# Optimization experiments

Measured on AMD Instinct MI355X. Metric: run time of the kernel, lower is better.

## Reference

```python
import jax, jax.numpy as jnp
import numpy as np
from jax import lax


def _conv(x, w, padding):
    # NCHW input, OIHW weights, stride 1, no bias
    return lax.conv_general_dilated(x, w, (1, 1), padding,
                                    dimension_numbers=('NCHW', 'OIHW', 'NCHW'))


def setup_inputs() -> dict:
    key = jax.random.key(0)
    ks = jax.random.split(key, 6)
    B, C, H, W = 16, 512, 40, 40
    return {
        'exemplar': jax.random.normal(ks[0], (B, C, H, W), jnp.float32),
        'query':    jax.random.normal(ks[1], (B, C, H, W), jnp.float32),
        'w_e':  jax.random.normal(ks[2], (256, C, 1, 1), jnp.float32) * 0.01,
        'w_q':  jax.random.normal(ks[3], (256, C, 1, 1), jnp.float32) * 0.01,
        'w_c1': jax.random.normal(ks[4], (C, C, 3, 3), jnp.float32) * 0.01,
        'w_c2': jax.random.normal(ks[5], (C, C, 3, 3), jnp.float32) * 0.01,
    }


def reference(exemplar, query, w_e, w_q, w_c1, w_c2):
    B, C, H, W = query.shape
    N = H * W
    # 1x1 projections to 256-dim correlation space
    q_corr = _conv(query, w_q, 'VALID').reshape(B, -1, N)     # [B,256,N]
    e_corr = _conv(exemplar, w_e, 'VALID').reshape(B, -1, N)  # [B,256,N]
    # A[b, n_exemplar, m_query] = <e_corr[:, n], q_corr[:, m]>
    A = jnp.einsum('bcn,bcm->bnm', e_corr, q_corr)            # [B,N,N]
    # A1 = softmax over exemplar axis, then transpose (torch: softmax(A,dim=1).T)
    A1 = jnp.swapaxes(jax.nn.softmax(A, axis=1), 1, 2)        # [B,N,N]
    # Bm = softmax(A^T, dim=1).T  == softmax(A, axis=2)
    Bm = jnp.swapaxes(jax.nn.softmax(jnp.swapaxes(A, 1, 2), axis=1), 1, 2)
    e_flat = exemplar.reshape(B, C, N)
    q_flat = query.reshape(B, C, N)
    query_att = jnp.matmul(e_flat, A1)   # [B,C,N]
    exemplar_att = jnp.matmul(q_flat, Bm)  # [B,C,N]
    input1_att = _conv(exemplar_att.reshape(B, C, H, W), w_c1, 'SAME')
    input2_att = _conv(query_att.reshape(B, C, H, W), w_c2, 'SAME')
    return jnp.concatenate([input1_att, input2_att], axis=1)  # [B,2C,H,W]
```

## Files before the change

kernel.cpp:

```cpp
#include <hip/hip_runtime.h>

typedef unsigned short u16;
typedef __attribute__((ext_vector_type(8))) short bf16x8;
typedef __attribute__((ext_vector_type(4))) float f32x4;

__device__ __forceinline__ u16 f2bf(float f) {
  union { float f; unsigned u; } v; v.f = f;
  unsigned u = v.u;
  u += 0x7fffu + ((u >> 16) & 1u);
  return (u16)(u >> 16);
}

__device__ __forceinline__ void gll16(const void* g, void* l) {
  __builtin_amdgcn_global_load_lds(
      (const __attribute__((address_space(1))) void*)g,
      (__attribute__((address_space(3))) void*)l, 16, 0, 0);
}

__global__ __launch_bounds__(256) void transp_cast_x2(const float* __restrict__ ex,
                                                      const float* __restrict__ qu,
                                                      u16* __restrict__ xte,
                                                      u16* __restrict__ xtq) {
  __shared__ float t[32][33];
  int z = blockIdx.z;
  int b = z & 15;
  const float* xb = (z < 16 ? ex : qu) + (size_t)b * 819200;
  u16* xtb = (z < 16 ? xte : xtq) + (size_t)b * 819200;
  int n0 = blockIdx.x * 32, c0 = blockIdx.y * 32;
  int tx = threadIdx.x & 31, ty = threadIdx.x >> 5;
#pragma unroll
  for (int k = 0; k < 4; k++) {
    int c = ty + k * 8;
    t[c][tx] = xb[(size_t)(c0 + c) * 1600 + n0 + tx];
  }
  __syncthreads();
#pragma unroll
  for (int k = 0; k < 4; k++) {
    int n = ty + k * 8;
    xtb[(size_t)(n0 + n) * 512 + c0 + tx] = f2bf(t[tx][n]);
  }
}

__global__ void cast_w(const float* __restrict__ we, const float* __restrict__ wq,
                       u16* __restrict__ oe, u16* __restrict__ oq) {
  int i = blockIdx.x * 256 + threadIdx.x;
  oe[i] = f2bf(we[i]);
  oq[i] = f2bf(wq[i]);
}

__global__ void repack_wc(const float* __restrict__ w1, const float* __restrict__ w2,
                          u16* __restrict__ o1, u16* __restrict__ o2) {
  const float* w = blockIdx.y ? w2 : w1;
  u16* wr = blockIdx.y ? o2 : o1;
  int idx = blockIdx.x * 256 + threadIdx.x;
  int o = idx / 4608;
  int r = idx - o * 4608;
  int t = r >> 9;
  int c = r & 511;
  wr[idx] = f2bf(w[o * 4608 + c * 9 + t]);
}

__global__ void zero_mem(uint4* __restrict__ p, long n) {
  long i = (long)blockIdx.x * blockDim.x + threadIdx.x;
  long stride = (long)gridDim.x * blockDim.x;
  uint4 z; z.x = 0; z.y = 0; z.z = 0; z.w = 0;
  for (; i < n; i += stride) p[i] = z;
}

template <int MODE>
__global__ __launch_bounds__(256) void gemm_bt64(
    const u16* __restrict__ A, const u16* __restrict__ B, u16* __restrict__ C,
    const u16* __restrict__ A2, const u16* __restrict__ B2, u16* __restrict__ C2,
    int M, int N, int K, long sA, long sB, long sC) {
  __shared__ u16 lds_a[128 * 64];
  __shared__ u16 lds_b[128 * 64];
  int tid = threadIdx.x;
  int z = blockIdx.z, b = z & 15;
  const u16* Ab = (z < 16 ? A : A2) + (size_t)b * sA;
  const u16* Bb = (z < 16 ? B : B2) + (size_t)b * sB;
  u16* Cb = (z < 16 ? C : C2) + (size_t)b * sC;
  int m0 = blockIdx.x * 128, n0 = blockIdx.y * 128;

  int rsub = tid >> 3;
  int gch = (tid & 7) ^ (rsub & 7);
  long Kb = (long)K * 2;
  const char* pa[4];
  const char* pb[4];
#pragma unroll
  for (int c = 0; c < 4; c++) {
    int ra = m0 + 32 * c + rsub; ra = ra < M ? ra : M - 1;
    int rb = n0 + 32 * c + rsub; rb = rb < N ? rb : N - 1;
    pa[c] = (const char*)Ab + (long)ra * Kb + gch * 16;
    pb[c] = (const char*)Bb + (long)rb * Kb + gch * 16;
  }

  const f32x4 fzero = {0.f, 0.f, 0.f, 0.f};
  f32x4 acc[4][4];
#pragma unroll
  for (int mi = 0; mi < 4; mi++)
#pragma unroll
    for (int ni = 0; ni < 4; ni++) acc[mi][ni] = fzero;

  int wid = tid >> 6, lane = tid & 63;
  int wm = wid & 1, wn = wid >> 1;
  int lrow = lane & 15, lquad = lane >> 4;
  int sl = lrow & 7;

  int ksteps = K >> 6;
  for (int ks = 0; ks < ksteps; ks++) {
#pragma unroll
    for (int c = 0; c < 4; c++) {
      gll16(pa[c], (char*)lds_a + c * 4096 + tid * 16);
      gll16(pb[c], (char*)lds_b + c * 4096 + tid * 16);
      pa[c] += 128; pb[c] += 128;
    }
    __syncthreads();
#pragma unroll
    for (int k2 = 0; k2 < 2; k2++) {
      int sel = ((k2 << 2) | lquad) ^ sl;
      bf16x8 bv[4];
#pragma unroll
      for (int ni = 0; ni < 4; ni++) {
        int rowb = wn * 64 + ni * 16 + lrow;
        bv[ni] = *(const bf16x8*)((const char*)lds_b + rowb * 128 + sel * 16);
      }
#pragma unroll
      for (int mi = 0; mi < 4; mi++) {
        int rowa = wm * 64 + mi * 16 + lrow;
        bf16x8 av = *(const bf16x8*)((const char*)lds_a + rowa * 128 + sel * 16);
#pragma unroll
        for (int ni = 0; ni < 4; ni++)
          acc[mi][ni] =
              __builtin_amdgcn_mfma_f32_16x16x32_bf16(av, bv[ni], acc[mi][ni], 0, 0, 0);
      }
    }
    __syncthreads();
  }

#pragma unroll
  for (int mi = 0; mi < 4; mi++) {
#pragma unroll
    for (int r = 0; r < 4; r++) {
      int i = m0 + wm * 64 + mi * 16 + lquad * 4 + r;
      if (i >= M) continue;
#pragma unroll
      for (int ni = 0; ni < 4; ni++) {
        int j = n0 + wn * 64 + ni * 16 + lrow;
        if (j >= N) continue;
        Cb[(size_t)i * N + j] = f2bf(acc[mi][ni][r]);
      }
    }
  }
}

__global__ __launch_bounds__(256) void gemm_corr_exp(
    const u16* __restrict__ A, const u16* __restrict__ B, u16* __restrict__ E,
    u16* __restrict__ ET, float* __restrict__ Zrow, float* __restrict__ Zcol) {
  __shared__ u16 lds_a[128 * 64];
  __shared__ u16 lds_b[128 * 64];
  int tid = threadIdx.x;
  int b = blockIdx.z;
  const u16* Ab = A + (size_t)b * 409600;
  const u16* Bb = B + (size_t)b * 409600;
  u16* Eb = E + (size_t)b * 2560000;
  u16* ETb = ET + (size_t)b * 2560000;
  int m0 = blockIdx.x * 128, n0 = blockIdx.y * 128;

  int rsub = tid >> 3;
  int gch = (tid & 7) ^ (rsub & 7);
  const char* pa[4];
  const char* pb[4];
#pragma unroll
  for (int c = 0; c < 4; c++) {
    int ra = m0 + 32 * c + rsub; ra = ra < 1600 ? ra : 1599;
    int rb = n0 + 32 * c + rsub; rb = rb < 1600 ? rb : 1599;
    pa[c] = (const char*)(Ab + (size_t)ra * 256) + gch * 16;
    pb[c] = (const char*)(Bb + (size_t)rb * 256) + gch * 16;
  }

  const f32x4 fzero = {0.f, 0.f, 0.f, 0.f};
  f32x4 acc[4][4];
#pragma unroll
  for (int mi = 0; mi < 4; mi++)
#pragma unroll
    for (int ni = 0; ni < 4; ni++) acc[mi][ni] = fzero;

  int wid = tid >> 6, lane = tid & 63;
  int wm = wid & 1, wn = wid >> 1;
  int lrow = lane & 15, lquad = lane >> 4;
  int sl = lrow & 7;

  for (int ks = 0; ks < 4; ks++) {
#pragma unroll
    for (int c = 0; c < 4; c++) {
      gll16(pa[c], (char*)lds_a + c * 4096 + tid * 16);
      gll16(pb[c], (char*)lds_b + c * 4096 + tid * 16);
      pa[c] += 128; pb[c] += 128;
    }
    __syncthreads();
#pragma unroll
    for (int k2 = 0; k2 < 2; k2++) {
      int sel = ((k2 << 2) | lquad) ^ sl;
      bf16x8 bv[4];
#pragma unroll
      for (int ni = 0; ni < 4; ni++) {
        int rowb = wn * 64 + ni * 16 + lrow;
        bv[ni] = *(const bf16x8*)((const char*)lds_b + rowb * 128 + sel * 16);
      }
#pragma unroll
      for (int mi = 0; mi < 4; mi++) {
        int rowa = wm * 64 + mi * 16 + lrow;
        bf16x8 av = *(const bf16x8*)((const char*)lds_a + rowa * 128 + sel * 16);
#pragma unroll
        for (int ni = 0; ni < 4; ni++)
          acc[mi][ni] =
              __builtin_amdgcn_mfma_f32_16x16x32_bf16(av, bv[ni], acc[mi][ni], 0, 0, 0);
      }
    }
    __syncthreads();
  }

  const int TS = 136;
  u16* T = lds_a;
  float colacc[4] = {0.f, 0.f, 0.f, 0.f};
#pragma unroll
  for (int s = 0; s < 4; s++) {
    if (wm == (s >> 1)) {
      int smi0 = (s & 1) * 2;
#pragma unroll
      for (int mi2 = 0; mi2 < 2; mi2++) {
        int mi = smi0 + mi2;
        float rowp[4] = {0.f, 0.f, 0.f, 0.f};
#pragma unroll
        for (int ni = 0; ni < 4; ni++) {
          int j = n0 + wn * 64 + ni * 16 + lrow;
          bool jv = j < 1600;
#pragma unroll
          for (int r = 0; r < 4; r++) {
            int i = m0 + wm * 64 + mi * 16 + lquad * 4 + r;
            float e = __expf(acc[mi][ni][r]);
            T[(mi2 * 16 + lquad * 4 + r) * TS + wn * 64 + ni * 16 + lrow] = f2bf(e);
            rowp[r] += jv ? e : 0.f;
            colacc[ni] += (i < 1600) ? e : 0.f;
          }
        }
#pragma unroll
        for (int r = 0; r < 4; r++) {
          float v = rowp[r];
          v += __shfl_xor(v, 1);
          v += __shfl_xor(v, 2);
          v += __shfl_xor(v, 4);
          v += __shfl_xor(v, 8);
          int i = m0 + wm * 64 + mi * 16 + lquad * 4 + r;
          if (lrow == 0 && i < 1600) atomicAdd(&Zrow[b * 1600 + i], v);
        }
      }
    }
    __syncthreads();
#pragma unroll
    for (int p = 0; p < 2; p++) {
      int jj = tid + p * 256;
      int ml = jj >> 4, n8 = jj & 15;
      int gi = m0 + s * 32 + ml, gj = n0 + n8 * 8;
      if (gi < 1600 && gj < 1600)
        *(uint4*)(Eb + (size_t)gi * 1600 + gj) = *(const uint4*)&T[ml * TS + n8 * 8];
    }
#pragma unroll
    for (int p = 0; p < 4; p++) {
      int jj = tid + p * 256;
      int n = jj >> 3, m4 = jj & 7;
      int gm = m0 + s * 32 + m4 * 4, gn = n0 + n;
      if (gn < 1600 && gm < 1600) {
        ushort4 v;
        v.x = T[(m4 * 4 + 0) * TS + n];
        v.y = T[(m4 * 4 + 1) * TS + n];
        v.z = T[(m4 * 4 + 2) * TS + n];
        v.w = T[(m4 * 4 + 3) * TS + n];
        *(ushort4*)(ETb + (size_t)gn * 1600 + gm) = v;
      }
    }
    __syncthreads();
  }
#pragma unroll
  for (int ni = 0; ni < 4; ni++) {
    float v = colacc[ni];
    v += __shfl_xor(v, 16);
    v += __shfl_xor(v, 32);
    int j = n0 + wn * 64 + ni * 16 + lrow;
    if (lquad == 0 && j < 1600) atomicAdd(&Zcol[b * 1600 + j], v);
  }
}

__global__ void scale_div(const float* __restrict__ ex, const float* __restrict__ qu,
                          const float* __restrict__ Zcol, const float* __restrict__ Zrow,
                          u16* __restrict__ ebf, u16* __restrict__ qbf) {
  const float* x; const float* Z; u16* o;
  if (blockIdx.y == 0) { x = ex; Z = Zcol; o = ebf; }
  else { x = qu; Z = Zrow; o = qbf; }
  size_t idx = (size_t)blockIdx.x * 256 + threadIdx.x;
  int b = (int)(idx / 819200);
  int i = (int)(idx % 1600);
  o[idx] = f2bf(x[idx] / Z[b * 1600 + i]);
}


__global__ __launch_bounds__(256, 2) void att_gemm128(
    const u16* __restrict__ Aw1, const u16* __restrict__ Bp1, u16* __restrict__ C1,
    const u16* __restrict__ Aw2, const u16* __restrict__ Bp2, u16* __restrict__ C2) {
  __shared__ u16 ldsA[16384];
  __shared__ u16 ldsB[16384];
  int tid = threadIdx.x;
  int flat = blockIdx.x + blockIdx.y * 13 + blockIdx.z * 52;
  int wrk = (flat & 7) * 208 + (flat >> 3);
  int z = wrk / 52;
  int r2 = wrk - z * 52;
  int by = r2 / 13, bx = r2 - by * 13;
  int b = z & 15;
  const u16* Aw = (z < 16 ? Aw1 : Aw2) + (size_t)b * 819200;
  const u16* Bp = (z < 16 ? Bp1 : Bp2) + (size_t)b * 2560000;
  u16* Cb = (z < 16 ? C1 : C2) + (size_t)b * 903168;
  int p0 = bx * 128, c0 = by * 128;

  int rl = tid >> 2;
  int cs = (tid & 3) ^ ((rl >> 1) & 3);
  const char* pA0 = (const char*)(Aw + (size_t)(c0 + rl) * 1600) + cs * 16;
  const char* pA1 = pA0 + 64 * 3200;
  int pp0 = p0 + rl; pp0 = pp0 < 1600 ? pp0 : 1599;
  const char* pB0 = (const char*)(Bp + (size_t)pp0 * 1600) + cs * 16;
  int pp1 = p0 + 64 + rl; pp1 = pp1 < 1600 ? pp1 : 1599;
  const char* pB1 = (const char*)(Bp + (size_t)pp1 * 1600) + cs * 16;

  char* ldsAb = (char*)ldsA;
  char* ldsBb = (char*)ldsB;
  int dstT = tid * 16;

#define STAGE_U(d, kh, ks)                                              \
  {                                                                     \
    int ko = (ks) * 64;                                                 \
    int ro = ((d) * 2 + (kh)) * 8192;                                   \
    gll16(pA0 + ko, ldsAb + ro + dstT);                                 \
    gll16(pA1 + ko, ldsAb + ro + 4096 + dstT);                          \
    gll16(pB0 + ko, ldsBb + ro + dstT);                                 \
    gll16(pB1 + ko, ldsBb + ro + 4096 + dstT);                          \
  }

  int wid = tid >> 6, lane = tid & 63;
  int wm = wid & 1, wn = wid >> 1;
  int lrow = lane & 15, lquad = lane >> 4;
  int csel = (lquad ^ ((lrow >> 1) & 3)) << 4;
  int aBase = (wm * 64 + lrow) * 64 + csel;
  int bBase = (wn * 64 + lrow) * 64 + csel;

  const f32x4 fzero = {0.f, 0.f, 0.f, 0.f};
  f32x4 acc[4][4];
#pragma unroll
  for (int mi = 0; mi < 4; mi++)
#pragma unroll
    for (int ni = 0; ni < 4; ni++) acc[mi][ni] = fzero;

  bf16x8 fa0, fa1, fa2, fa3, fb0, fb1, fb2, fb3;
  bf16x8 ga0, ga1, ga2, ga3, gb0, gb1, gb2, gb3;

#define RD(pre, d, kh)                                                  \
  {                                                                     \
    const char* ra_ = ldsAb + ((d) * 2 + (kh)) * 8192 + aBase;          \
    const char* rb_ = ldsBb + ((d) * 2 + (kh)) * 8192 + bBase;          \
    pre##a0 = *(const bf16x8*)(ra_);                                    \
    pre##a1 = *(const bf16x8*)(ra_ + 1024);                             \
    pre##a2 = *(const bf16x8*)(ra_ + 2048);                             \
    pre##a3 = *(const bf16x8*)(ra_ + 3072);                             \
    pre##b0 = *(const bf16x8*)(rb_);                                    \
    pre##b1 = *(const bf16x8*)(rb_ + 1024);                             \
    pre##b2 = *(const bf16x8*)(rb_ + 2048);                             \
    pre##b3 = *(const bf16x8*)(rb_ + 3072);                             \
  }

#define MROW(mi, av, pre)                                                               \
  acc[mi][0] = __builtin_amdgcn_mfma_f32_16x16x32_bf16(av, pre##b0, acc[mi][0], 0, 0, 0); \
  acc[mi][1] = __builtin_amdgcn_mfma_f32_16x16x32_bf16(av, pre##b1, acc[mi][1], 0, 0, 0); \
  acc[mi][2] = __builtin_amdgcn_mfma_f32_16x16x32_bf16(av, pre##b2, acc[mi][2], 0, 0, 0); \
  acc[mi][3] = __builtin_amdgcn_mfma_f32_16x16x32_bf16(av, pre##b3, acc[mi][3], 0, 0, 0);

#define MALL(pre)                                                              \
  MROW(0, pre##a0, pre) MROW(1, pre##a1, pre) MROW(2, pre##a2, pre) MROW(3, pre##a3, pre)

#define PHASE(rd_d, rd_kh, rdp, cp, STG)                                       \
  {                                                                            \
    STG;                                                                       \
    asm volatile("s_waitcnt vmcnt(4)" ::: "memory");                           \
    __builtin_amdgcn_s_barrier();                                              \
    RD(rdp, rd_d, rd_kh);                                                      \
    __builtin_amdgcn_s_setprio(1);                                             \
    MALL(cp)                                                                   \
    __builtin_amdgcn_s_setprio(0);                                             \
  }

  STAGE_U(0, 0, 0);
  STAGE_U(0, 1, 1);
  asm volatile("s_waitcnt vmcnt(4)" ::: "memory");
  __builtin_amdgcn_s_barrier();
  RD(f, 0, 0);

#pragma unroll 1
  for (int it = 0; it < 12; ++it) {
    int k2 = it * 4 + 2, k3 = it * 4 + 3, k4 = it * 4 + 4, k5 = it * 4 + 5;
    PHASE(0, 1, g, f, STAGE_U(1, 0, k2));
    PHASE(1, 0, f, g, STAGE_U(1, 1, k3));
    PHASE(1, 1, g, f, STAGE_U(0, 0, k4));
    PHASE(0, 0, f, g, STAGE_U(0, 1, k5));
  }
  asm volatile("s_waitcnt vmcnt(0)" ::: "memory");
  __builtin_amdgcn_s_barrier();
  RD(g, 0, 1);
  __builtin_amdgcn_s_setprio(1);
  MALL(f)
  MALL(g)
  __builtin_amdgcn_s_setprio(0);

#undef PHASE
#undef MALL
#undef MROW
#undef RD
#undef STAGE_U

#pragma unroll
  for (int mi = 0; mi < 4; mi++) {
#pragma unroll
    for (int r = 0; r < 4; r++) {
      int o = c0 + wm * 64 + mi * 16 + lquad * 4 + r;
#pragma unroll
      for (int ni = 0; ni < 4; ni++) {
        int p = p0 + wn * 64 + ni * 16 + lrow;
        if (p < 1600) {
          int y = p / 40, x = p - y * 40;
          Cb[(size_t)((y + 1) * 42 + (x + 1)) * 512 + o] = f2bf(acc[mi][ni][r]);
        }
      }
    }
  }
}

__global__ __launch_bounds__(256, 2) void conv_gemm128(
    const u16* __restrict__ W1, const u16* __restrict__ ATT1,
    const u16* __restrict__ W2, const u16* __restrict__ ATT2,
    float* __restrict__ out) {
  __shared__ u16 ldsA[16384];
  __shared__ u16 ldsB[16384];
  int tid = threadIdx.x;
  int flat = blockIdx.x + blockIdx.y * 13 + blockIdx.z * 52;
  int wrk = (flat & 7) * 208 + (flat >> 3);
  int z = wrk / 52;
  int r2 = wrk - z * 52;
  int by = r2 / 13, bx = r2 - by * 13;
  int b = z & 15, sel2 = z >> 4;
  const u16* W = sel2 ? W2 : W1;
  const u16* attb = (sel2 ? ATT2 : ATT1) + (size_t)b * 903168;
  float* outb = out + (size_t)b * 1638400 + (size_t)(sel2 ? 512 : 0) * 1600;
  int p0 = bx * 128, o0 = by * 128;

  int rl = tid >> 2;
  int cs = (tid & 3) ^ ((rl >> 1) & 3);
  const char* pA0 = (const char*)(W + (size_t)(o0 + rl) * 4608) + cs * 16;
  const char* pA1 = pA0 + 64 * 9216;
  int pp0 = p0 + rl; pp0 = pp0 < 1600 ? pp0 : 1599;
  int y0 = pp0 / 40, x0 = pp0 - y0 * 40;
  const char* pB0 = (const char*)(attb + (size_t)(y0 * 42 + x0) * 512) + cs * 16;
  int pp1 = p0 + 64 + rl; pp1 = pp1 < 1600 ? pp1 : 1599;
  int y1 = pp1 / 40, x1 = pp1 - y1 * 40;
  const char* pB1 = (const char*)(attb + (size_t)(y1 * 42 + x1) * 512) + cs * 16;

  char* ldsAb = (char*)ldsA;
  char* ldsBb = (char*)ldsB;
  int dstT = tid * 16;

#define STAGE_U(d, kh, ks)                                              \
  {                                                                     \
    int koA = (ks) * 64;                                                \
    int tp = (ks) >> 4;                                                 \
    int ty = (tp * 11) >> 5;                                            \
    int tx = tp - ty * 3;                                               \
    int koB = (ty * 42 + tx) * 1024 + ((ks) & 15) * 64;                 \
    int ro = ((d) * 2 + (kh)) * 8192;                                   \
    gll16(pA0 + koA, ldsAb + ro + dstT);                                \
    gll16(pA1 + koA, ldsAb + ro + 4096 + dstT);                         \
    gll16(pB0 + koB, ldsBb + ro + dstT);                                \
    gll16(pB1 + koB, ldsBb + ro + 4096 + dstT);                         \
  }

  int wid = tid >> 6, lane = tid & 63;
  int wm = wid & 1, wn = wid >> 1;
  int lrow = lane & 15, lquad = lane >> 4;
  int csel = (lquad ^ ((lrow >> 1) & 3)) << 4;
  int aBase = (wm * 64 + lrow) * 64 + csel;
  int bBase = (wn * 64 + lrow) * 64 + csel;

  const f32x4 fzero = {0.f, 0.f, 0.f, 0.f};
  f32x4 acc[4][4];
#pragma unroll
  for (int mi = 0; mi < 4; mi++)
#pragma unroll
    for (int ni = 0; ni < 4; ni++) acc[mi][ni] = fzero;

  bf16x8 fa0, fa1, fa2, fa3, fb0, fb1, fb2, fb3;
  bf16x8 ga0, ga1, ga2, ga3, gb0, gb1, gb2, gb3;

#define RD(pre, d, kh)                                                  \
  {                                                                     \
    const char* ra_ = ldsAb + ((d) * 2 + (kh)) * 8192 + aBase;          \
    const char* rb_ = ldsBb + ((d) * 2 + (kh)) * 8192 + bBase;          \
    pre##a0 = *(const bf16x8*)(ra_);                                    \
    pre##a1 = *(const bf16x8*)(ra_ + 1024);                             \
    pre##a2 = *(const bf16x8*)(ra_ + 2048);                             \
    pre##a3 = *(const bf16x8*)(ra_ + 3072);                             \
    pre##b0 = *(const bf16x8*)(rb_);                                    \
    pre##b1 = *(const bf16x8*)(rb_ + 1024);                             \
    pre##b2 = *(const bf16x8*)(rb_ + 2048);                             \
    pre##b3 = *(const bf16x8*)(rb_ + 3072);                             \
  }

#define MROW(mi, av, pre)                                                               \
  acc[mi][0] = __builtin_amdgcn_mfma_f32_16x16x32_bf16(av, pre##b0, acc[mi][0], 0, 0, 0); \
  acc[mi][1] = __builtin_amdgcn_mfma_f32_16x16x32_bf16(av, pre##b1, acc[mi][1], 0, 0, 0); \
  acc[mi][2] = __builtin_amdgcn_mfma_f32_16x16x32_bf16(av, pre##b2, acc[mi][2], 0, 0, 0); \
  acc[mi][3] = __builtin_amdgcn_mfma_f32_16x16x32_bf16(av, pre##b3, acc[mi][3], 0, 0, 0);

#define MALL(pre)                                                              \
  MROW(0, pre##a0, pre) MROW(1, pre##a1, pre) MROW(2, pre##a2, pre) MROW(3, pre##a3, pre)

#define PHASE(rd_d, rd_kh, rdp, cp, STG)                                       \
  {                                                                            \
    STG;                                                                       \
    asm volatile("s_waitcnt vmcnt(4)" ::: "memory");                           \
    __builtin_amdgcn_s_barrier();                                              \
    RD(rdp, rd_d, rd_kh);                                                      \
    __builtin_amdgcn_s_setprio(1);                                             \
    MALL(cp)                                                                   \
    __builtin_amdgcn_s_setprio(0);                                             \
  }

  STAGE_U(0, 0, 0);
  STAGE_U(0, 1, 1);
  asm volatile("s_waitcnt vmcnt(4)" ::: "memory");
  __builtin_amdgcn_s_barrier();
  RD(f, 0, 0);

#pragma unroll 1
  for (int it = 0; it < 36; ++it) {
    int k2 = it * 4 + 2, k3 = it * 4 + 3;
    int k4 = it * 4 + 4; k4 = k4 < 144 ? k4 : 143;
    int k5 = it * 4 + 5; k5 = k5 < 144 ? k5 : 143;
    PHASE(0, 1, g, f, STAGE_U(1, 0, k2));
    PHASE(1, 0, f, g, STAGE_U(1, 1, k3));
    PHASE(1, 1, g, f, STAGE_U(0, 0, k4));
    PHASE(0, 0, f, g, STAGE_U(0, 1, k5));
  }

#undef PHASE
#undef MALL
#undef MROW
#undef RD
#undef STAGE_U

#pragma unroll
  for (int mi = 0; mi < 4; mi++) {
#pragma unroll
    for (int r = 0; r < 4; r++) {
      int o = o0 + wm * 64 + mi * 16 + lquad * 4 + r;
      float* orow = outb + (size_t)o * 1600;
#pragma unroll
      for (int ni = 0; ni < 4; ni++) {
        int p = p0 + wn * 64 + ni * 16 + lrow;
        if (p < 1600) orow[p] = acc[mi][ni][r];
      }
    }
  }
}

extern "C" void kernel_launch(void* const* d_in, const int* in_sizes, int n_in,
                              void* d_out, int out_size, void* d_ws, size_t ws_size,
                              hipStream_t stream) {
  const float* ex = (const float*)d_in[0];
  const float* qu = (const float*)d_in[1];
  const float* w_e = (const float*)d_in[2];
  const float* w_q = (const float*)d_in[3];
  const float* w_c1 = (const float*)d_in[4];
  const float* w_c2 = (const float*)d_in[5];
  float* out = (float*)d_out;
  char* ws = (char*)d_ws;

  u16* E     = (u16*)(ws + 0L);
  u16* ET    = (u16*)(ws + 81920000L);
  u16* xt_e  = (u16*)(ws + 163840000L);
  u16* xt_q  = (u16*)(ws + 190054400L);
  u16* ecorr = (u16*)(ws + 216268800L);
  u16* qcorr = (u16*)(ws + 229376000L);
  u16* att_e = (u16*)(ws + 242483200L);
  u16* att_q = (u16*)(ws + 271384576L);
  float* Zrow = (float*)(ws + 300285952L);
  float* Zcol = (float*)(ws + 300388352L);
  u16* w_ebf = (u16*)(ws + 300490752L);
  u16* w_qbf = (u16*)(ws + 300752896L);
  u16* wr1   = (u16*)(ws + 301015040L);
  u16* wr2   = (u16*)(ws + 305733632L);

  transp_cast_x2<<<dim3(50, 16, 32), 256, 0, stream>>>(ex, qu, xt_e, xt_q);
  cast_w<<<dim3(512), 256, 0, stream>>>(w_e, w_q, w_ebf, w_qbf);
  repack_wc<<<dim3(9216, 2), 256, 0, stream>>>(w_c1, w_c2, wr1, wr2);
  zero_mem<<<dim3(2048), 256, 0, stream>>>((uint4*)att_e, 3625472L);

  gemm_bt64<0><<<dim3(13, 2, 32), 256, 0, stream>>>(
      xt_e, w_ebf, ecorr, xt_q, w_qbf, qcorr, 1600, 256, 512, 819200L, 0L, 409600L);

  gemm_corr_exp<<<dim3(13, 13, 16), 256, 0, stream>>>(ecorr, qcorr, E, ET, Zrow, Zcol);

  u16* ebf = xt_e;
  u16* qbf = xt_q;
  scale_div<<<dim3(51200, 2), 256, 0, stream>>>(ex, qu, Zcol, Zrow, ebf, qbf);

  att_gemm128<<<dim3(13, 4, 32), 256, 0, stream>>>(ebf, E, att_q, qbf, ET, att_e);

  conv_gemm128<<<dim3(13, 4, 32), 256, 0, stream>>>(wr1, att_e, wr2, att_q, out);
}
```

Before: 882.5 us.

## Pipeline projection/corr GEMMs, enlarge conv tile, zero only padding borders

```diff
diff --git a/kernel.cpp b/kernel.cpp
--- a/kernel.cpp
+++ b/kernel.cpp
@@ -60,168 +60,276 @@
   wr[idx] = f2bf(w[o * 4608 + c * 9 + t]);
 }
 
-__global__ void zero_mem(uint4* __restrict__ p, long n) {
-  long i = (long)blockIdx.x * blockDim.x + threadIdx.x;
-  long stride = (long)gridDim.x * blockDim.x;
-  uint4 z; z.x = 0; z.y = 0; z.z = 0; z.w = 0;
-  for (; i < n; i += stride) p[i] = z;
-}
-
-template <int MODE>
-__global__ __launch_bounds__(256) void gemm_bt64(
-    const u16* __restrict__ A, const u16* __restrict__ B, u16* __restrict__ C,
-    const u16* __restrict__ A2, const u16* __restrict__ B2, u16* __restrict__ C2,
-    int M, int N, int K, long sA, long sB, long sC) {
-  __shared__ u16 lds_a[128 * 64];
-  __shared__ u16 lds_b[128 * 64];
+__global__ void zero_pad(u16* __restrict__ att, float* __restrict__ Z) {
+  int q = blockIdx.x;
+  uint4 zz; zz.x = 0; zz.y = 0; zz.z = 0; zz.w = 0;
+  if (q < 32) {
+    uint4* base = (uint4*)(att + (size_t)q * 903168);
+    for (int i = threadIdx.x; i < 10496; i += 256) {
+      int t = i >> 6, c = i & 63;
+      int y, x;
+      if (t < 42) { y = 0; x = t; }
+      else if (t < 84) { y = 41; x = t - 42; }
+      else if (t < 124) { y = 1 + (t - 84); x = 0; }
+      else { y = 1 + (t - 124); x = 41; }
+      base[(y * 42 + x) * 64 + c] = zz;
+    }
+  } else {
+    uint4* p = (uint4*)Z;
+    for (int i = threadIdx.x; i < 12800; i += 256) p[i] = zz;
+  }
+}
+
+
+__global__ __launch_bounds__(256, 2) void corr_gemm128(
+    const u16* __restrict__ X1, const u16* __restrict__ Wg1, u16* __restrict__ C1,
+    const u16* __restrict__ X2, const u16* __restrict__ Wg2, u16* __restrict__ C2) {
+  __shared__ u16 ldsA[16384];
+  __shared__ u16 ldsB[16384];
   int tid = threadIdx.x;
-  int z = blockIdx.z, b = z & 15;
-  const u16* Ab = (z < 16 ? A : A2) + (size_t)b * sA;
-  const u16* Bb = (z < 16 ? B : B2) + (size_t)b * sB;
-  u16* Cb = (z < 16 ? C : C2) + (size_t)b * sC;
-  int m0 = blockIdx.x * 128, n0 = blockIdx.y * 128;
-
-  int rsub = tid >> 3;
-  int gch = (tid & 7) ^ (rsub & 7);
-  long Kb = (long)K * 2;
-  const char* pa[4];
-  const char* pb[4];
-#pragma unroll
-  for (int c = 0; c < 4; c++) {
-    int ra = m0 + 32 * c + rsub; ra = ra < M ? ra : M - 1;
-    int rb = n0 + 32 * c + rsub; rb = rb < N ? rb : N - 1;
-    pa[c] = (const char*)Ab + (long)ra * Kb + gch * 16;
-    pb[c] = (const char*)Bb + (long)rb * Kb + gch * 16;
-  }
-
-  const f32x4 fzero = {0.f, 0.f, 0.f, 0.f};
-  f32x4 acc[4][4];
-#pragma unroll
-  for (int mi = 0; mi < 4; mi++)
-#pragma unroll
-    for (int ni = 0; ni < 4; ni++) acc[mi][ni] = fzero;
+  int flat = blockIdx.x + blockIdx.y * 13 + blockIdx.z * 26;
+  int wrk = (flat & 7) * 104 + (flat >> 3);
+  int z = wrk / 26;
+  int r2 = wrk - z * 26;
+  int by = r2 / 13, bx = r2 - by * 13;
+  int b = z & 15;
+  const u16* A = (z < 16 ? X1 : X2) + (size_t)b * 819200;
+  const u16* B = (z < 16 ? Wg1 : Wg2);
+  u16* Cb = (z < 16 ? C1 : C2) + (size_t)b * 409600;
+  int m0 = bx * 128, n0 = by * 128;
+
+  int rl = tid >> 2;
+  int cs = (tid & 3) ^ ((rl >> 1) & 3);
+  int ra0 = m0 + rl; ra0 = ra0 < 1600 ? ra0 : 1599;
+  int ra1 = m0 + 64 + rl; ra1 = ra1 < 1600 ? ra1 : 1599;
+  const char* pA0 = (const char*)(A + (size_t)ra0 * 512) + cs * 16;
+  const char* pA1 = (const char*)(A + (size_t)ra1 * 512) + cs * 16;
+  const char* pB0 = (const char*)(B + (size_t)(n0 + rl) * 512) + cs * 16;
+  const char* pB1 = (const char*)(B + (size_t)(n0 + 64 + rl) * 512) + cs * 16;
+
+  char* ldsAb = (char*)ldsA;
+  char* ldsBb = (char*)ldsB;
+  int dstT = tid * 16;
+
+#define STAGE_U(d, kh, ks)                                              \
+  {                                                                     \
+    int ko = (ks) * 64;                                                 \
+    int ro = ((d) * 2 + (kh)) * 8192;                                   \
+    gll16(pA0 + ko, ldsAb + ro + dstT);                                 \
+    gll16(pA1 + ko, ldsAb + ro + 4096 + dstT);                          \
+    gll16(pB0 + ko, ldsBb + ro + dstT);                                 \
+    gll16(pB1 + ko, ldsBb + ro + 4096 + dstT);                          \
+  }
 
   int wid = tid >> 6, lane = tid & 63;
   int wm = wid & 1, wn = wid >> 1;
   int lrow = lane & 15, lquad = lane >> 4;
-  int sl = lrow & 7;
-
-  int ksteps = K >> 6;
-  for (int ks = 0; ks < ksteps; ks++) {
-#pragma unroll
-    for (int c = 0; c < 4; c++) {
-      gll16(pa[c], (char*)lds_a + c * 4096 + tid * 16);
-      gll16(pb[c], (char*)lds_b + c * 4096 + tid * 16);
-      pa[c] += 128; pb[c] += 128;
-    }
-    __syncthreads();
-#pragma unroll
-    for (int k2 = 0; k2 < 2; k2++) {
-      int sel = ((k2 << 2) | lquad) ^ sl;
-      bf16x8 bv[4];
+  int csel = (lquad ^ ((lrow >> 1) & 3)) << 4;
+  int aBase = (wm * 64 + lrow) * 64 + csel;
+  int bBase = (wn * 64 + lrow) * 64 + csel;
+
+  const f32x4 fzero = {0.f, 0.f, 0.f, 0.f};
+  f32x4 acc[4][4];
+#pragma unroll
+  for (int mi = 0; mi < 4; mi++)
+#pragma unroll
+    for (int ni = 0; ni < 4; ni++) acc[mi][ni] = fzero;
+
+  bf16x8 fa0, fa1, fa2, fa3, fb0, fb1, fb2, fb3;
+  bf16x8 ga0, ga1, ga2, ga3, gb0, gb1, gb2, gb3;
+
+#define RD(pre, d, kh)                                                  \
+  {                                                                     \
+    const char* ra_ = ldsAb + ((d) * 2 + (kh)) * 8192 + aBase;          \
+    const char* rb_ = ldsBb + ((d) * 2 + (kh)) * 8192 + bBase;          \
+    pre##a0 = *(const bf16x8*)(ra_);                                    \
+    pre##a1 = *(const bf16x8*)(ra_ + 1024);                             \
+    pre##a2 = *(const bf16x8*)(ra_ + 2048);                             \
+    pre##a3 = *(const bf16x8*)(ra_ + 3072);                             \
+    pre##b0 = *(const bf16x8*)(rb_);                                    \
+    pre##b1 = *(const bf16x8*)(rb_ + 1024);                             \
+    pre##b2 = *(const bf16x8*)(rb_ + 2048);                             \
+    pre##b3 = *(const bf16x8*)(rb_ + 3072);                             \
+  }
+
+#define MROW(mi, av, pre)                                                               \
+  acc[mi][0] = __builtin_amdgcn_mfma_f32_16x16x32_bf16(av, pre##b0, acc[mi][0], 0, 0, 0); \
+  acc[mi][1] = __builtin_amdgcn_mfma_f32_16x16x32_bf16(av, pre##b1, acc[mi][1], 0, 0, 0); \
+  acc[mi][2] = __builtin_amdgcn_mfma_f32_16x16x32_bf16(av, pre##b2, acc[mi][2], 0, 0, 0); \
+  acc[mi][3] = __builtin_amdgcn_mfma_f32_16x16x32_bf16(av, pre##b3, acc[mi][3], 0, 0, 0);
+
+#define MALL(pre)                                                              \
+  MROW(0, pre##a0, pre) MROW(1, pre##a1, pre) MROW(2, pre##a2, pre) MROW(3, pre##a3, pre)
+
+#define PHASE(rd_d, rd_kh, rdp, cp, STG)                                       \
+  {                                                                            \
+    STG;                                                                       \
+    asm volatile("s_waitcnt vmcnt(4)" ::: "memory");                           \
+    __builtin_amdgcn_s_barrier();                                              \
+    RD(rdp, rd_d, rd_kh);                                                      \
+    __builtin_amdgcn_s_setprio(1);                                             \
+    MALL(cp)                                                                   \
+    __builtin_amdgcn_s_setprio(0);                                             \
+  }
+
+  STAGE_U(0, 0, 0);
+  STAGE_U(0, 1, 1);
+  asm volatile("s_waitcnt vmcnt(4)" ::: "memory");
+  __builtin_amdgcn_s_barrier();
+  RD(f, 0, 0);
+
+#pragma unroll 1
+  for (int it = 0; it < 4; ++it) {
+    int k2 = it * 4 + 2, k3 = it * 4 + 3;
+    int k4 = it * 4 + 4; k4 = k4 < 16 ? k4 : 15;
+    int k5 = it * 4 + 5; k5 = k5 < 16 ? k5 : 15;
+    PHASE(0, 1, g, f, STAGE_U(1, 0, k2));
+    PHASE(1, 0, f, g, STAGE_U(1, 1, k3));
+    PHASE(1, 1, g, f, STAGE_U(0, 0, k4));
+    PHASE(0, 0, f, g, STAGE_U(0, 1, k5));
+  }
+
+#undef PHASE
+#undef MALL
+#undef MROW
+#undef RD
+#undef STAGE_U
+
+#pragma unroll
+  for (int mi = 0; mi < 4; mi++) {
+#pragma unroll
+    for (int r = 0; r < 4; r++) {
+      int i = m0 + wm * 64 + mi * 16 + lquad * 4 + r;
+      if (i >= 1600) continue;
 #pragma unroll
       for (int ni = 0; ni < 4; ni++) {
-        int rowb = wn * 64 + ni * 16 + lrow;
-        bv[ni] = *(const bf16x8*)((const char*)lds_b + rowb * 128 + sel * 16);
-      }
-#pragma unroll
-      for (int mi = 0; mi < 4; mi++) {
-        int rowa = wm * 64 + mi * 16 + lrow;
-        bf16x8 av = *(const bf16x8*)((const char*)lds_a + rowa * 128 + sel * 16);
-#pragma unroll
-        for (int ni = 0; ni < 4; ni++)
-          acc[mi][ni] =
-              __builtin_amdgcn_mfma_f32_16x16x32_bf16(av, bv[ni], acc[mi][ni], 0, 0, 0);
+        int j = n0 + wn * 64 + ni * 16 + lrow;
+        Cb[(size_t)i * 256 + j] = f2bf(acc[mi][ni][r]);
       }
     }
-    __syncthreads();
-  }
-
-#pragma unroll
-  for (int mi = 0; mi < 4; mi++) {
-#pragma unroll
-    for (int r = 0; r < 4; r++) {
-      int i = m0 + wm * 64 + mi * 16 + lquad * 4 + r;
-      if (i >= M) continue;
-#pragma unroll
-      for (int ni = 0; ni < 4; ni++) {
-        int j = n0 + wn * 64 + ni * 16 + lrow;
-        if (j >= N) continue;
-        Cb[(size_t)i * N + j] = f2bf(acc[mi][ni][r]);
-      }
-    }
-  }
-}
-
-__global__ __launch_bounds__(256) void gemm_corr_exp(
+  }
+}
+
+__global__ __launch_bounds__(256, 2) void corr_exp128(
     const u16* __restrict__ A, const u16* __restrict__ B, u16* __restrict__ E,
     u16* __restrict__ ET, float* __restrict__ Zrow, float* __restrict__ Zcol) {
-  __shared__ u16 lds_a[128 * 64];
-  __shared__ u16 lds_b[128 * 64];
+  __shared__ u16 ldsA[16384];
+  __shared__ u16 ldsB[16384];
   int tid = threadIdx.x;
-  int b = blockIdx.z;
+  int flat = blockIdx.x + blockIdx.y * 13 + blockIdx.z * 169;
+  int wrk = (flat & 7) * 338 + (flat >> 3);
+  int b = wrk / 169;
+  int r2 = wrk - b * 169;
+  int by = r2 / 13, bx = r2 - by * 13;
   const u16* Ab = A + (size_t)b * 409600;
   const u16* Bb = B + (size_t)b * 409600;
   u16* Eb = E + (size_t)b * 2560000;
   u16* ETb = ET + (size_t)b * 2560000;
-  int m0 = blockIdx.x * 128, n0 = blockIdx.y * 128;
-
-  int rsub = tid >> 3;
-  int gch = (tid & 7) ^ (rsub & 7);
-  const char* pa[4];
-  const char* pb[4];
-#pragma unroll
-  for (int c = 0; c < 4; c++) {
-    int ra = m0 + 32 * c + rsub; ra = ra < 1600 ? ra : 1599;
-    int rb = n0 + 32 * c + rsub; rb = rb < 1600 ? rb : 1599;
-    pa[c] = (const char*)(Ab + (size_t)ra * 256) + gch * 16;
-    pb[c] = (const char*)(Bb + (size_t)rb * 256) + gch * 16;
-  }
-
-  const f32x4 fzero = {0.f, 0.f, 0.f, 0.f};
-  f32x4 acc[4][4];
-#pragma unroll
-  for (int mi = 0; mi < 4; mi++)
-#pragma unroll
-    for (int ni = 0; ni < 4; ni++) acc[mi][ni] = fzero;
+  int m0 = bx * 128, n0 = by * 128;
+
+  int rl = tid >> 2;
+  int cs = (tid & 3) ^ ((rl >> 1) & 3);
+  int ra0 = m0 + rl; ra0 = ra0 < 1600 ? ra0 : 1599;
+  int ra1 = m0 + 64 + rl; ra1 = ra1 < 1600 ? ra1 : 1599;
+  int rb0 = n0 + rl; rb0 = rb0 < 1600 ? rb0 : 1599;
+  int rb1 = n0 + 64 + rl; rb1 = rb1 < 1600 ? rb1 : 1599;
+  const char* pA0 = (const char*)(Ab + (size_t)ra0 * 256) + cs * 16;
+  const char* pA1 = (const char*)(Ab + (size_t)ra1 * 256) + cs * 16;
+  const char* pB0 = (const char*)(Bb + (size_t)rb0 * 256) + cs * 16;
+  const char* pB1 = (const char*)(Bb + (size_t)rb1 * 256) + cs * 16;
+
+  char* ldsAb = (char*)ldsA;
+  char* ldsBb = (char*)ldsB;
+  int dstT = tid * 16;
+
+#define STAGE_U(d, kh, ks)                                              \
+  {                                                                     \
+    int ko = (ks) * 64;                                                 \
+    int ro = ((d) * 2 + (kh)) * 8192;                                   \
+    gll16(pA0 + ko, ldsAb + ro + dstT);                                 \
+    gll16(pA1 + ko, ldsAb + ro + 4096 + dstT);                          \
+    gll16(pB0 + ko, ldsBb + ro + dstT);                                 \
+    gll16(pB1 + ko, ldsBb + ro + 4096 + dstT);                          \
+  }
 
   int wid = tid >> 6, lane = tid & 63;
   int wm = wid & 1, wn = wid >> 1;
   int lrow = lane & 15, lquad = lane >> 4;
-  int sl = lrow & 7;
-
-  for (int ks = 0; ks < 4; ks++) {
-#pragma unroll
-    for (int c = 0; c < 4; c++) {
-      gll16(pa[c], (char*)lds_a + c * 4096 + tid * 16);
-      gll16(pb[c], (char*)lds_b + c * 4096 + tid * 16);
-      pa[c] += 128; pb[c] += 128;
-    }
-    __syncthreads();
-#pragma unroll
-    for (int k2 = 0; k2 < 2; k2++) {
-      int sel = ((k2 << 2) | lquad) ^ sl;
-      bf16x8 bv[4];
-#pragma unroll
-      for (int ni = 0; ni < 4; ni++) {
-        int rowb = wn * 64 + ni * 16 + lrow;
-        bv[ni] = *(const bf16x8*)((const char*)lds_b + rowb * 128 + sel * 16);
-      }
-#pragma unroll
-      for (int mi = 0; mi < 4; mi++) {
-        int rowa = wm * 64 + mi * 16 + lrow;
-        bf16x8 av = *(const bf16x8*)((const char*)lds_a + rowa * 128 + sel * 16);
-#pragma unroll
-        for (int ni = 0; ni < 4; ni++)
-          acc[mi][ni] =
-              __builtin_amdgcn_mfma_f32_16x16x32_bf16(av, bv[ni], acc[mi][ni], 0, 0, 0);
-      }
-    }
-    __syncthreads();
-  }
+  int csel = (lquad ^ ((lrow >> 1) & 3)) << 4;
+  int aBase = (wm * 64 + lrow) * 64 + csel;
+  int bBase = (wn * 64 + lrow) * 64 + csel;
+
+  const f32x4 fzero = {0.f, 0.f, 0.f, 0.f};
+  f32x4 acc[4][4];
+#pragma unroll
+  for (int mi = 0; mi < 4; mi++)
+#pragma unroll
+    for (int ni = 0; ni < 4; ni++) acc[mi][ni] = fzero;
+
+  bf16x8 fa0, fa1, fa2, fa3, fb0, fb1, fb2, fb3;
+  bf16x8 ga0, ga1, ga2, ga3, gb0, gb1, gb2, gb3;
+
+#define RD(pre, d, kh)                                                  \
+  {                                                                     \
+    const char* ra_ = ldsAb + ((d) * 2 + (kh)) * 8192 + aBase;          \
+    const char* rb_ = ldsBb + ((d) * 2 + (kh)) * 8192 + bBase;          \
+    pre##a0 = *(const bf16x8*)(ra_);                                    \
+    pre##a1 = *(const bf16x8*)(ra_ + 1024);                             \
+    pre##a2 = *(const bf16x8*)(ra_ + 2048);                             \
+    pre##a3 = *(const bf16x8*)(ra_ + 3072);                             \
+    pre##b0 = *(const bf16x8*)(rb_);                                    \
+    pre##b1 = *(const bf16x8*)(rb_ + 1024);                             \
+    pre##b2 = *(const bf16x8*)(rb_ + 2048);                             \
+    pre##b3 = *(const bf16x8*)(rb_ + 3072);                             \
+  }
+
+#define MROW(mi, av, pre)                                                               \
+  acc[mi][0] = __builtin_amdgcn_mfma_f32_16x16x32_bf16(av, pre##b0, acc[mi][0], 0, 0, 0); \
+  acc[mi][1] = __builtin_amdgcn_mfma_f32_16x16x32_bf16(av, pre##b1, acc[mi][1], 0, 0, 0); \
+  acc[mi][2] = __builtin_amdgcn_mfma_f32_16x16x32_bf16(av, pre##b2, acc[mi][2], 0, 0, 0); \
+  acc[mi][3] = __builtin_amdgcn_mfma_f32_16x16x32_bf16(av, pre##b3, acc[mi][3], 0, 0, 0);
+
+#define MALL(pre)                                                              \
+  MROW(0, pre##a0, pre) MROW(1, pre##a1, pre) MROW(2, pre##a2, pre) MROW(3, pre##a3, pre)
+
+#define PHASE(rd_d, rd_kh, rdp, cp, STG)                                       \
+  {                                                                            \
+    STG;                                                                       \
+    asm volatile("s_waitcnt vmcnt(4)" ::: "memory");                           \
+    __builtin_amdgcn_s_barrier();                                              \
+    RD(rdp, rd_d, rd_kh);                                                      \
+    __builtin_amdgcn_s_setprio(1);                                             \
+    MALL(cp)                                                                   \
+    __builtin_amdgcn_s_setprio(0);                                             \
+  }
+
+  STAGE_U(0, 0, 0);
+  STAGE_U(0, 1, 1);
+  asm volatile("s_waitcnt vmcnt(4)" ::: "memory");
+  __builtin_amdgcn_s_barrier();
+  RD(f, 0, 0);
+
+#pragma unroll 1
+  for (int it = 0; it < 2; ++it) {
+    int k2 = it * 4 + 2, k3 = it * 4 + 3;
+    int k4 = it * 4 + 4; k4 = k4 < 8 ? k4 : 7;
+    int k5 = it * 4 + 5; k5 = k5 < 8 ? k5 : 7;
+    PHASE(0, 1, g, f, STAGE_U(1, 0, k2));
+    PHASE(1, 0, f, g, STAGE_U(1, 1, k3));
+    PHASE(1, 1, g, f, STAGE_U(0, 0, k4));
+    PHASE(0, 0, f, g, STAGE_U(0, 1, k5));
+  }
+
+#undef PHASE
+#undef MALL
+#undef MROW
+#undef RD
+#undef STAGE_U
+
+  __syncthreads();
 
   const int TS = 136;
-  u16* T = lds_a;
+  u16* T = ldsA;
   float colacc[4] = {0.f, 0.f, 0.f, 0.f};
 #pragma unroll
   for (int s = 0; s < 4; s++) {
@@ -302,7 +410,6 @@
   int i = (int)(idx % 1600);
   o[idx] = f2bf(x[idx] / Z[b * 1600 + i]);
 }
-
 
 __global__ __launch_bounds__(256, 2) void att_gemm128(
     const u16* __restrict__ Aw1, const u16* __restrict__ Bp1, u16* __restrict__ C1,
@@ -440,32 +547,27 @@
   }
 }
 
-__global__ __launch_bounds__(256, 2) void conv_gemm128(
+__global__ __launch_bounds__(512, 2) void conv_gemmpf(
     const u16* __restrict__ W1, const u16* __restrict__ ATT1,
     const u16* __restrict__ W2, const u16* __restrict__ ATT2,
     float* __restrict__ out) {
-  __shared__ u16 ldsA[16384];
-  __shared__ u16 ldsB[16384];
+  __shared__ u16 ldsA[32768];
+  __shared__ u16 ldsB[32768];
   int tid = threadIdx.x;
-  int flat = blockIdx.x + blockIdx.y * 13 + blockIdx.z * 52;
-  int wrk = (flat & 7) * 208 + (flat >> 3);
-  int z = wrk / 52;
-  int r2 = wrk - z * 52;
-  int by = r2 / 13, bx = r2 - by * 13;
-  int b = z & 15, sel2 = z >> 4;
+  int z = blockIdx.z, b = z & 15, sel2 = z >> 4;
   const u16* W = sel2 ? W2 : W1;
   const u16* attb = (sel2 ? ATT2 : ATT1) + (size_t)b * 903168;
   float* outb = out + (size_t)b * 1638400 + (size_t)(sel2 ? 512 : 0) * 1600;
-  int p0 = bx * 128, o0 = by * 128;
+  int p0 = blockIdx.x * 224, o0 = blockIdx.y * 256;
 
   int rl = tid >> 2;
   int cs = (tid & 3) ^ ((rl >> 1) & 3);
   const char* pA0 = (const char*)(W + (size_t)(o0 + rl) * 4608) + cs * 16;
-  const char* pA1 = pA0 + 64 * 9216;
+  const char* pA1 = pA0 + 128 * 9216;
   int pp0 = p0 + rl; pp0 = pp0 < 1600 ? pp0 : 1599;
   int y0 = pp0 / 40, x0 = pp0 - y0 * 40;
   const char* pB0 = (const char*)(attb + (size_t)(y0 * 42 + x0) * 512) + cs * 16;
-  int pp1 = p0 + 64 + rl; pp1 = pp1 < 1600 ? pp1 : 1599;
+  int pp1 = p0 + 128 + rl; pp1 = pp1 < 1600 ? pp1 : 1599;
   int y1 = pp1 / 40, x1 = pp1 - y1 * 40;
   const char* pB1 = (const char*)(attb + (size_t)(y1 * 42 + x1) * 512) + cs * 16;
 
@@ -473,41 +575,44 @@
   char* ldsBb = (char*)ldsB;
   int dstT = tid * 16;
 
-#define STAGE_U(d, kh, ks)                                              \
-  {                                                                     \
-    int koA = (ks) * 64;                                                \
-    int tp = (ks) >> 4;                                                 \
+#define STAGE_A(d, kh, kt)                                              \
+  {                                                                     \
+    int ko = (kt) * 128 + (kh) * 64;                                    \
+    gll16(pA0 + ko, ldsAb + ((d) * 2 + (kh)) * 16384 + dstT);           \
+    gll16(pA1 + ko, ldsAb + ((d) * 2 + (kh)) * 16384 + 8192 + dstT);    \
+  }
+#define STAGE_B(d, kh, kt)                                              \
+  {                                                                     \
+    int tp = (kt) >> 3;                                                 \
     int ty = (tp * 11) >> 5;                                            \
     int tx = tp - ty * 3;                                               \
-    int koB = (ty * 42 + tx) * 1024 + ((ks) & 15) * 64;                 \
-    int ro = ((d) * 2 + (kh)) * 8192;                                   \
-    gll16(pA0 + koA, ldsAb + ro + dstT);                                \
-    gll16(pA1 + koA, ldsAb + ro + 4096 + dstT);                         \
-    gll16(pB0 + koB, ldsBb + ro + dstT);                                \
-    gll16(pB1 + koB, ldsBb + ro + 4096 + dstT);                         \
-  }
+    int ko = (ty * 42 + tx) * 1024 + ((kt) & 7) * 128 + (kh) * 64;      \
+    gll16(pB0 + ko, ldsBb + ((d) * 2 + (kh)) * 16384 + dstT);           \
+    gll16(pB1 + ko, ldsBb + ((d) * 2 + (kh)) * 16384 + 8192 + dstT);    \
+  }
+#define STAGE_U(d, kh, kt) { STAGE_A(d, kh, kt); STAGE_B(d, kh, kt); }
 
   int wid = tid >> 6, lane = tid & 63;
-  int wm = wid & 1, wn = wid >> 1;
+  int wm = wid & 3, wn = wid >> 2;
   int lrow = lane & 15, lquad = lane >> 4;
   int csel = (lquad ^ ((lrow >> 1) & 3)) << 4;
   int aBase = (wm * 64 + lrow) * 64 + csel;
-  int bBase = (wn * 64 + lrow) * 64 + csel;
+  int bBase = (wn * 112 + lrow) * 64 + csel;
 
   const f32x4 fzero = {0.f, 0.f, 0.f, 0.f};
-  f32x4 acc[4][4];
+  f32x4 acc[4][7];
 #pragma unroll
   for (int mi = 0; mi < 4; mi++)
 #pragma unroll
-    for (int ni = 0; ni < 4; ni++) acc[mi][ni] = fzero;
-
-  bf16x8 fa0, fa1, fa2, fa3, fb0, fb1, fb2, fb3;
-  bf16x8 ga0, ga1, ga2, ga3, gb0, gb1, gb2, gb3;
+    for (int ni = 0; ni < 7; ni++) acc[mi][ni] = fzero;
+
+  bf16x8 fa0, fa1, fa2, fa3, fb0, fb1, fb2, fb3, fb4, fb5, fb6;
+  bf16x8 ga0, ga1, ga2, ga3, gb0, gb1, gb2, gb3, gb4, gb5, gb6;
 
 #define RD(pre, d, kh)                                                  \
   {                                                                     \
-    const char* ra_ = ldsAb + ((d) * 2 + (kh)) * 8192 + aBase;          \
-    const char* rb_ = ldsBb + ((d) * 2 + (kh)) * 8192 + bBase;          \
+    const char* ra_ = ldsAb + ((d) * 2 + (kh)) * 16384 + aBase;         \
+    const char* rb_ = ldsBb + ((d) * 2 + (kh)) * 16384 + bBase;         \
     pre##a0 = *(const bf16x8*)(ra_);                                    \
     pre##a1 = *(const bf16x8*)(ra_ + 1024);                             \
     pre##a2 = *(const bf16x8*)(ra_ + 2048);                             \
@@ -516,16 +621,19 @@
     pre##b1 = *(const bf16x8*)(rb_ + 1024);                             \
     pre##b2 = *(const bf16x8*)(rb_ + 2048);                             \
     pre##b3 = *(const bf16x8*)(rb_ + 3072);                             \
+    pre##b4 = *(const bf16x8*)(rb_ + 4096);                             \
+    pre##b5 = *(const bf16x8*)(rb_ + 5120);                             \
+    pre##b6 = *(const bf16x8*)(rb_ + 6144);                             \
   }
 
 #define MROW(mi, av, pre)                                                               \
   acc[mi][0] = __builtin_amdgcn_mfma_f32_16x16x32_bf16(av, pre##b0, acc[mi][0], 0, 0, 0); \
   acc[mi][1] = __builtin_amdgcn_mfma_f32_16x16x32_bf16(av, pre##b1, acc[mi][1], 0, 0, 0); \
   acc[mi][2] = __builtin_amdgcn_mfma_f32_16x16x32_bf16(av, pre##b2, acc[mi][2], 0, 0, 0); \
-  acc[mi][3] = __builtin_amdgcn_mfma_f32_16x16x32_bf16(av, pre##b3, acc[mi][3], 0, 0, 0);
-
-#define MALL(pre)                                                              \
-  MROW(0, pre##a0, pre) MROW(1, pre##a1, pre) MROW(2, pre##a2, pre) MROW(3, pre##a3, pre)
+  acc[mi][3] = __builtin_amdgcn_mfma_f32_16x16x32_bf16(av, pre##b3, acc[mi][3], 0, 0, 0); \
+  acc[mi][4] = __builtin_amdgcn_mfma_f32_16x16x32_bf16(av, pre##b4, acc[mi][4], 0, 0, 0); \
+  acc[mi][5] = __builtin_amdgcn_mfma_f32_16x16x32_bf16(av, pre##b5, acc[mi][5], 0, 0, 0); \
+  acc[mi][6] = __builtin_amdgcn_mfma_f32_16x16x32_bf16(av, pre##b6, acc[mi][6], 0, 0, 0);
 
 #define PHASE(rd_d, rd_kh, rdp, cp, STG)                                       \
   {                                                                            \
@@ -534,32 +642,35 @@
     __builtin_amdgcn_s_barrier();                                              \
     RD(rdp, rd_d, rd_kh);                                                      \
     __builtin_amdgcn_s_setprio(1);                                             \
-    MALL(cp)                                                                   \
+    MROW(0, cp##a0, cp)                                                        \
+    MROW(1, cp##a1, cp)                                                        \
+    MROW(2, cp##a2, cp)                                                        \
+    MROW(3, cp##a3, cp)                                                        \
     __builtin_amdgcn_s_setprio(0);                                             \
   }
 
   STAGE_U(0, 0, 0);
-  STAGE_U(0, 1, 1);
+  STAGE_U(0, 1, 0);
   asm volatile("s_waitcnt vmcnt(4)" ::: "memory");
   __builtin_amdgcn_s_barrier();
   RD(f, 0, 0);
 
 #pragma unroll 1
   for (int it = 0; it < 36; ++it) {
-    int k2 = it * 4 + 2, k3 = it * 4 + 3;
-    int k4 = it * 4 + 4; k4 = k4 < 144 ? k4 : 143;
-    int k5 = it * 4 + 5; k5 = k5 < 144 ? k5 : 143;
-    PHASE(0, 1, g, f, STAGE_U(1, 0, k2));
-    PHASE(1, 0, f, g, STAGE_U(1, 1, k3));
-    PHASE(1, 1, g, f, STAGE_U(0, 0, k4));
-    PHASE(0, 0, f, g, STAGE_U(0, 1, k5));
+    int kt1 = it * 2 + 1;
+    int kt2 = it < 35 ? it * 2 + 2 : 71;
+    PHASE(0, 1, g, f, STAGE_U(1, 0, kt1));
+    PHASE(1, 0, f, g, STAGE_U(1, 1, kt1));
+    PHASE(1, 1, g, f, STAGE_U(0, 0, kt2));
+    PHASE(0, 0, f, g, STAGE_U(0, 1, kt2));
   }
 
 #undef PHASE
-#undef MALL
 #undef MROW
 #undef RD
 #undef STAGE_U
+#undef STAGE_A
+#undef STAGE_B
 
 #pragma unroll
   for (int mi = 0; mi < 4; mi++) {
@@ -568,8 +679,8 @@
       int o = o0 + wm * 64 + mi * 16 + lquad * 4 + r;
       float* orow = outb + (size_t)o * 1600;
 #pragma unroll
-      for (int ni = 0; ni < 4; ni++) {
-        int p = p0 + wn * 64 + ni * 16 + lrow;
+      for (int ni = 0; ni < 7; ni++) {
+        int p = p0 + wn * 112 + ni * 16 + lrow;
         if (p < 1600) orow[p] = acc[mi][ni][r];
       }
     }
@@ -606,12 +717,12 @@
   transp_cast_x2<<<dim3(50, 16, 32), 256, 0, stream>>>(ex, qu, xt_e, xt_q);
   cast_w<<<dim3(512), 256, 0, stream>>>(w_e, w_q, w_ebf, w_qbf);
   repack_wc<<<dim3(9216, 2), 256, 0, stream>>>(w_c1, w_c2, wr1, wr2);
-  zero_mem<<<dim3(2048), 256, 0, stream>>>((uint4*)att_e, 3625472L);
-
-  gemm_bt64<0><<<dim3(13, 2, 32), 256, 0, stream>>>(
-      xt_e, w_ebf, ecorr, xt_q, w_qbf, qcorr, 1600, 256, 512, 819200L, 0L, 409600L);
-
-  gemm_corr_exp<<<dim3(13, 13, 16), 256, 0, stream>>>(ecorr, qcorr, E, ET, Zrow, Zcol);
+  zero_pad<<<dim3(33), 256, 0, stream>>>(att_e, Zrow);
+
+  corr_gemm128<<<dim3(13, 2, 32), 256, 0, stream>>>(
+      xt_e, w_ebf, ecorr, xt_q, w_qbf, qcorr);
+
+  corr_exp128<<<dim3(13, 13, 16), 256, 0, stream>>>(ecorr, qcorr, E, ET, Zrow, Zcol);
 
   u16* ebf = xt_e;
   u16* qbf = xt_q;
@@ -619,5 +730,5 @@
 
   att_gemm128<<<dim3(13, 4, 32), 256, 0, stream>>>(ebf, E, att_q, qbf, ET, att_e);
 
-  conv_gemm128<<<dim3(13, 4, 32), 256, 0, stream>>>(wr1, att_e, wr2, att_q, out);
-}
+  conv_gemmpf<<<dim3(8, 2, 32), 512, 0, stream>>>(wr1, att_e, wr2, att_q, out);
+}
```

Result: faster. 796.1 us (-9.8%).
